# Kernel tuning notes

Hardware: AMD Instinct MI355X
Metric: run time of the kernel (lower is better)

Reference implementation:

```python
import jax, jax.numpy as jnp
import numpy as np

# sigmas (defaults from the module)
VAR_0, VAR_A, VAR_B = 1.0, 1.0, 0.0

def V_phi(a, b, c):
    # default id_phi: (a, b, c) -> b, where Sigma = [[a, b], [b, c]]
    return b


def setup_inputs() -> dict:
    key = jax.random.key(0)
    kx, ky = jax.random.split(key)
    B, T, D = 128, 1024, 64
    dt = 1.0 / (T - 1)
    scale = np.sqrt(dt / D).astype(np.float32)
    # Brownian-like paths: increments ~ N(0, dt/D) so quadratic variation is O(1)
    # and the multiplicative kernel recurrence stays numerically bounded.
    X = jnp.cumsum(jax.random.normal(kx, (B, T, D), jnp.float32) * scale, axis=1)
    Y = jnp.cumsum(jax.random.normal(ky, (B, T, D), jnp.float32) * scale, axis=1)
    return {"X": X, "Y": Y}


def _kernel_same(dd):
    # dd: (b, T-1) = <dX_t, dX_t> / dt ; returns Kxx: (b, T)
    def step(k, d_t):
        k_new = k + (VAR_A * V_phi(k, k, k) + VAR_B) * d_t
        return k_new, k_new
    k0 = jnp.full((dd.shape[0],), VAR_0, dd.dtype)
    _, ks = jax.lax.scan(step, k0, dd.T)           # ks: (T-1, b)
    return jnp.concatenate([k0[None, :], ks], axis=0).T  # (b, T)


def reference(X, Y):
    bx, T, d = X.shape
    by = Y.shape[0]
    interval = jnp.linspace(0.0, 1.0, T).astype(X.dtype)
    dt = jnp.diff(interval)                         # (T-1,)
    dX = jnp.diff(X, axis=1)                        # (bx, T-1, d)
    dY = jnp.diff(Y, axis=1)                        # (by, T-1, d)

    dXdX = (dX * dX).sum(-1) / dt                   # (bx, T-1)
    dYdY = (dY * dY).sum(-1) / dt                   # (by, T-1)
    dXdY = jnp.einsum('itd,jtd->ijt', dX, dY) / dt  # (bx, by, T-1)

    Kxx = _kernel_same(dXdX)                        # (bx, T)
    Kyy = _kernel_same(dYdY)                        # (by, T)

    def step(k, inp):
        kxx_t, kyy_t, dxy_t = inp                   # (bx,), (by,), (bx, by)
        k_new = k + (VAR_A * V_phi(kxx_t[:, None], k, kyy_t[None, :]) + VAR_B) * dxy_t
        return k_new, k_new

    k0 = jnp.full((bx, by), VAR_0, X.dtype)
    xs = (Kxx[:, :-1].T, Kyy[:, :-1].T, jnp.moveaxis(dXdY, 2, 0))
    _, ks = jax.lax.scan(step, k0, xs)              # (T-1, bx, by)
    K = jnp.concatenate([k0[None], ks], axis=0)     # (T, bx, by)
    return jnp.moveaxis(K, 0, 2)                    # (bx, by, T)
```

## Files before the change

### kernel.cpp

```cpp
#include <hip/hip_runtime.h>
#include <hip/hip_bf16.h>

typedef __attribute__((ext_vector_type(8))) short short8;
typedef __attribute__((ext_vector_type(4))) float floatx4;

constexpr int BX    = 128;
constexpr int TT    = 1024;
constexpr int DDIM  = 64;
constexpr int NPAIR = BX * BX;
constexpr int LCH   = 16;
constexpr int NCH   = TT / LCH;
constexpr float DT_INV = 1023.0f;

__device__ __forceinline__ int sidxE(int row, int k) {
    return row * 64 + ((((k >> 3) ^ (row & 7)) << 3) | (k & 7));
}

__device__ __forceinline__ ushort f2bf(float f) {
    uint u = __builtin_bit_cast(uint, f);
    u += 0x7fffu + ((u >> 16) & 1u);
    return (ushort)(u >> 16);
}

__device__ __forceinline__ void cvt_store(ushort* hiP, ushort* loP, const float* v) {
    uint hw[4], lw[4];
#pragma unroll
    for (int p = 0; p < 4; ++p) {
        const __hip_bfloat162 h = __float22bfloat162_rn(make_float2(v[2 * p], v[2 * p + 1]));
        const float r0 = v[2 * p]     - __bfloat162float(h.x);
        const float r1 = v[2 * p + 1] - __bfloat162float(h.y);
        const __hip_bfloat162 l = __float22bfloat162_rn(make_float2(r0, r1));
        hw[p] = (uint)__bfloat16_as_ushort(h.x) | ((uint)__bfloat16_as_ushort(h.y) << 16);
        lw[p] = (uint)__bfloat16_as_ushort(l.x) | ((uint)__bfloat16_as_ushort(l.y) << 16);
    }
    *(uint4*)hiP = make_uint4(hw[0], hw[1], hw[2], hw[3]);
    *(uint4*)loP = make_uint4(lw[0], lw[1], lw[2], lw[3]);
}

__device__ __forceinline__ void ld8(const float* p, float* dst) {
    const float4 a = *(const float4*)p;
    const float4 b = *(const float4*)(p + 4);
    dst[0] = a.x; dst[1] = a.y; dst[2] = a.z; dst[3] = a.w;
    dst[4] = b.x; dst[5] = b.y; dst[6] = b.z; dst[7] = b.w;
}

template<int WP>
__global__ __launch_bounds__(256, 2) void zchunk_kernel(const float* __restrict__ X,
                                                        const float* __restrict__ Y,
                                                        float* __restrict__ dstF,
                                                        uint*  __restrict__ Wp,
                                                        float* __restrict__ P)
{
    __shared__ __align__(16) ushort smXhi[2][64 * 64], smXlo[2][64 * 64];
    __shared__ __align__(16) ushort smYhi[2][32 * 64], smYlo[2][32 * 64];

    const int L    = (int)blockIdx.x;
    const int tile = (L >> 3) & 7;
    const int cz   = ((L >> 6) << 3) | (L & 7);
    const int i0 = (tile & 1) * 64;
    const int j0 = (tile >> 1) * 32;
    const int t0 = cz * LCH;
    const int tid  = (int)threadIdx.x;
    const int lane = tid & 63, w = tid >> 6, quad = lane >> 4, l15 = lane & 15;

    const int srow = tid >> 3;
    const int sseg = tid & 7;
    const float* xp0 = X + (size_t)(i0 + srow)      * TT * DDIM + sseg * 8;
    const float* xp1 = X + (size_t)(i0 + srow + 32) * TT * DDIM + sseg * 8;
    const float* yp  = Y + (size_t)(j0 + srow)      * TT * DDIM + sseg * 8;

    float cx0[8], cx1[8], cy[8];
    float rx0[4][8], rx1[4][8], ry[4][8];
    {
        const int sa = (t0 == 0) ? 0 : (t0 - 1);
        float pv0[8], pv1[8], pv2[8], d[8];
        ld8(xp0 + (size_t)t0 * DDIM, cx0);
        ld8(xp1 + (size_t)t0 * DDIM, cx1);
        ld8(yp  + (size_t)t0 * DDIM, cy);
        ld8(xp0 + (size_t)sa * DDIM, pv0);
        ld8(xp1 + (size_t)sa * DDIM, pv1);
        ld8(yp  + (size_t)sa * DDIM, pv2);
#pragma unroll
        for (int s = 1; s <= 3; ++s) {
            ld8(xp0 + (size_t)(t0 + s) * DDIM, rx0[s]);
            ld8(xp1 + (size_t)(t0 + s) * DDIM, rx1[s]);
            ld8(yp  + (size_t)(t0 + s) * DDIM, ry[s]);
        }

#pragma unroll
        for (int k = 0; k < 8; ++k) d[k] = cx0[k] - pv0[k];
        cvt_store(&smXhi[0][sidxE(srow, sseg * 8)], &smXlo[0][sidxE(srow, sseg * 8)], d);
#pragma unroll
        for (int k = 0; k < 8; ++k) d[k] = cx1[k] - pv1[k];
        cvt_store(&smXhi[0][sidxE(srow + 32, sseg * 8)], &smXlo[0][sidxE(srow + 32, sseg * 8)], d);
#pragma unroll
        for (int k = 0; k < 8; ++k) d[k] = cy[k] - pv2[k];
        cvt_store(&smYhi[0][sidxE(srow, sseg * 8)], &smYlo[0][sidxE(srow, sseg * 8)], d);
    }

    float cum[2][4];
    uint  histP[2][4][8];
#pragma unroll
    for (int s = 0; s < 2; ++s)
#pragma unroll
        for (int r = 0; r < 4; ++r) cum[s][r] = 1.f;

    __syncthreads();

#pragma unroll
    for (int h = 0; h < LCH; ++h) {
        const int cur = h & 1;

        if (h + 4 < LCH) {
            const size_t u = (size_t)(t0 + h + 4) * DDIM;
            ld8(xp0 + u, rx0[h & 3]); ld8(xp1 + u, rx1[h & 3]); ld8(yp + u, ry[h & 3]);
        }

        short8 aHi[2], aLo[2];
#pragma unroll
        for (int kk = 0; kk < 2; ++kk) {
            const int e = sidxE(w * 16 + l15, kk * 32 + quad * 8);
            aHi[kk] = *(const short8*)&smXhi[cur][e];
            aLo[kk] = *(const short8*)&smXlo[cur][e];
        }

#pragma unroll
        for (int sub = 0; sub < 2; ++sub) {
            floatx4 acc = {0.f, 0.f, 0.f, 0.f};
#pragma unroll
            for (int kk = 0; kk < 2; ++kk) {
                const int e = sidxE(sub * 16 + l15, kk * 32 + quad * 8);
                const short8 bHi = *(const short8*)&smYhi[cur][e];
                const short8 bLo = *(const short8*)&smYlo[cur][e];
                acc = __builtin_amdgcn_mfma_f32_16x16x32_bf16(aLo[kk], bHi, acc, 0, 0, 0);
                acc = __builtin_amdgcn_mfma_f32_16x16x32_bf16(aHi[kk], bLo, acc, 0, 0, 0);
                acc = __builtin_amdgcn_mfma_f32_16x16x32_bf16(aHi[kk], bHi, acc, 0, 0, 0);
            }
#pragma unroll
            for (int r = 0; r < 4; ++r) {
                cum[sub][r] *= fmaf(acc[r], DT_INV, 1.f);
                const uint hb = (uint)f2bf(cum[sub][r]);
                if ((h & 1) == 0) histP[sub][r][h >> 1] = hb;
                else              histP[sub][r][h >> 1] |= (hb << 16);
            }
        }

        if (h + 1 < LCH) {
            const int nsel = (h + 1) & 3;
            float d[8];
#pragma unroll
            for (int k = 0; k < 8; ++k) d[k] = rx0[nsel][k] - cx0[k];
            cvt_store(&smXhi[cur ^ 1][sidxE(srow, sseg * 8)], &smXlo[cur ^ 1][sidxE(srow, sseg * 8)], d);
#pragma unroll
            for (int k = 0; k < 8; ++k) d[k] = rx1[nsel][k] - cx1[k];
            cvt_store(&smXhi[cur ^ 1][sidxE(srow + 32, sseg * 8)], &smXlo[cur ^ 1][sidxE(srow + 32, sseg * 8)], d);
#pragma unroll
            for (int k = 0; k < 8; ++k) d[k] = ry[nsel][k] - cy[k];
            cvt_store(&smYhi[cur ^ 1][sidxE(srow, sseg * 8)], &smYlo[cur ^ 1][sidxE(srow, sseg * 8)], d);
#pragma unroll
            for (int k = 0; k < 8; ++k) { cx0[k] = rx0[nsel][k]; cx1[k] = rx1[nsel][k]; cy[k] = ry[nsel][k]; }
            __syncthreads();
        }
    }

#pragma unroll
    for (int sub = 0; sub < 2; ++sub)
#pragma unroll
        for (int r = 0; r < 4; ++r) {
            const int pair = (i0 + w * 16 + quad * 4 + r) * BX + (j0 + sub * 16 + l15);
            P[(size_t)cz * NPAIR + pair] = cum[sub][r];
            if (WP) {
                uint* o = Wp + ((size_t)cz * NPAIR + pair) * 8;
                *(uint4*)o       = make_uint4(histP[sub][r][0], histP[sub][r][1],
                                              histP[sub][r][2], histP[sub][r][3]);
                *(uint4*)(o + 4) = make_uint4(histP[sub][r][4], histP[sub][r][5],
                                              histP[sub][r][6], histP[sub][r][7]);
            } else {
                float* o = dstF + (size_t)pair * TT + t0;
#pragma unroll
                for (int q = 0; q < 4; ++q) {
                    const uint u0 = histP[sub][r][2 * q];
                    const uint u1 = histP[sub][r][2 * q + 1];
                    *(float4*)(o + q * 4) = make_float4(
                        __builtin_bit_cast(float, u0 << 16),
                        __builtin_bit_cast(float, u0 & 0xffff0000u),
                        __builtin_bit_cast(float, u1 << 16),
                        __builtin_bit_cast(float, u1 & 0xffff0000u));
                }
            }
        }
}

__global__ __launch_bounds__(256) void scanscale_w(float* __restrict__ out,
                                                   const uint* __restrict__ W,
                                                   const float* __restrict__ P)
{
    __shared__ uint2 tileW[NCH * 65];
    __shared__ float pf[NCH][17];
    __shared__ float tot[16][17];

    const int p0  = (int)blockIdx.x * 16;
    const int tid = (int)threadIdx.x;
    const int p   = tid & 15;
    const int seg = tid >> 4;

    float v[4], e[4];
#pragma unroll
    for (int k = 0; k < 4; ++k)
        v[k] = P[(size_t)(seg * 4 + k) * NPAIR + p0 + p];
    e[0] = 1.f;
#pragma unroll
    for (int k = 1; k < 4; ++k) e[k] = e[k - 1] * v[k - 1];
    tot[seg][p] = e[3] * v[3];
    __syncthreads();

    float base = 1.f;
#pragma unroll
    for (int q = 0; q < 15; ++q)
        if (q < seg) base *= tot[q][p];
#pragma unroll
    for (int k = 0; k < 4; ++k)
        pf[seg * 4 + k][p] = base * e[k];

    const int wv = tid >> 6, l = tid & 63;
    const int pr = l >> 2, tb = l & 3;
#pragma unroll
    for (int k = 0; k < 16; ++k) {
        const int c = wv * 16 + k;
        tileW[c * 65 + pr * 4 + tb] =
            *(const uint2*)(W + ((size_t)c * NPAIR + p0 + pr) * 8 + tb * 2);
    }
    __syncthreads();

    const int c2 = tid >> 2, q2 = tid & 3;
#pragma unroll 2
    for (int r = 0; r < 16; ++r) {
        const uint2 u = tileW[c2 * 65 + r * 4 + q2];
        const float f = pf[c2][r];
        *(float4*)(out + (size_t)(p0 + r) * TT + tid * 4) = make_float4(
            __builtin_bit_cast(float, u.x << 16) * f,
            __builtin_bit_cast(float, u.x & 0xffff0000u) * f,
            __builtin_bit_cast(float, u.y << 16) * f,
            __builtin_bit_cast(float, u.y & 0xffff0000u) * f);
    }
}

__global__ __launch_bounds__(256) void scanscale_kernel(float* __restrict__ out,
                                                        const float* __restrict__ P)
{
    __shared__ float pf[16][NCH];
    const int p0  = (int)blockIdx.x * 16;
    const int tid = (int)threadIdx.x;

    if (tid < 16) {
        const int p = p0 + tid;
        float run = 1.f;
#pragma unroll 4
        for (int c = 0; c < NCH; ++c) {
            pf[tid][c] = run;
            run *= P[(size_t)c * NPAIR + p];
        }
    }
    __syncthreads();

    const int pp  = tid >> 4;
    const int col = tid & 15;
    float* row = out + (size_t)(p0 + pp) * TT;
#pragma unroll
    for (int seg = 0; seg < 16; ++seg) {
        const int t = seg * 64 + col * 4;
        const float f = pf[pp][t >> 4];
        float4 v = *(float4*)(row + t);
        v.x *= f; v.y *= f; v.z *= f; v.w *= f;
        *(float4*)(row + t) = v;
    }
}

extern "C" void kernel_launch(void* const* d_in, const int* in_sizes, int n_in,
                              void* d_out, int out_size, void* d_ws, size_t ws_size,
                              hipStream_t stream)
{
    const float* X = (const float*)d_in[0];
    const float* Y = (const float*)d_in[1];
    float* out = (float*)d_out;
    float* P   = (float*)d_ws;
    uint*  W   = (uint*)((float*)d_ws + (size_t)NCH * NPAIR);

    const size_t need = (size_t)NCH * NPAIR * (4 + 32);
    if (ws_size >= need) {
        zchunk_kernel<1><<<dim3(512), 256, 0, stream>>>(X, Y, out, W, P);
        scanscale_w<<<dim3(NPAIR / 16), 256, 0, stream>>>(out, W, P);
    } else {
        zchunk_kernel<0><<<dim3(512), 256, 0, stream>>>(X, Y, out, W, P);
        scanscale_kernel<<<dim3(NPAIR / 16), 256, 0, stream>>>(out, P);
    }
}
```

Baseline: 149.0 us.

## Split chunk kernel into single-wave 16x16 tiles without block barriers

Replaces the 256-thread chunk kernel computing 64x32 pair tiles with a one-wavefront kernel computing 16x16 tiles, launched as 4096 blocks. With one wave per block the LDS double buffer no longer needs __syncthreads, and the prefetch depth drops from 4 to 2 steps to save registers. The aim is more parallel blocks and no barrier stalls, at the cost of less reuse of the X/Y increments per tile and so more global/L2 traffic.

```diff
diff --git a/kernel.cpp b/kernel.cpp
--- a/kernel.cpp
+++ b/kernel.cpp
@@ -45,150 +45,152 @@
 }
 
 template<int WP>
-__global__ __launch_bounds__(256, 2) void zchunk_kernel(const float* __restrict__ X,
-                                                        const float* __restrict__ Y,
-                                                        float* __restrict__ dstF,
-                                                        uint*  __restrict__ Wp,
-                                                        float* __restrict__ P)
-{
-    __shared__ __align__(16) ushort smXhi[2][64 * 64], smXlo[2][64 * 64];
-    __shared__ __align__(16) ushort smYhi[2][32 * 64], smYlo[2][32 * 64];
+__global__ __launch_bounds__(64, 2) void zchunk1w(const float* __restrict__ X,
+                                                  const float* __restrict__ Y,
+                                                  float* __restrict__ dstF,
+                                                  uint*  __restrict__ Wp,
+                                                  float* __restrict__ P)
+{
+    __shared__ __align__(16) ushort smXhi[2][16 * 64], smXlo[2][16 * 64];
+    __shared__ __align__(16) ushort smYhi[2][16 * 64], smYlo[2][16 * 64];
 
     const int L    = (int)blockIdx.x;
-    const int tile = (L >> 3) & 7;
-    const int cz   = ((L >> 6) << 3) | (L & 7);
-    const int i0 = (tile & 1) * 64;
-    const int j0 = (tile >> 1) * 32;
+    const int tile = (L >> 3) & 63;
+    const int cz   = ((L >> 9) << 3) | (L & 7);
+    const int i0 = (tile & 7) * 16;
+    const int j0 = (tile >> 3) * 16;
     const int t0 = cz * LCH;
-    const int tid  = (int)threadIdx.x;
-    const int lane = tid & 63, w = tid >> 6, quad = lane >> 4, l15 = lane & 15;
-
-    const int srow = tid >> 3;
-    const int sseg = tid & 7;
-    const float* xp0 = X + (size_t)(i0 + srow)      * TT * DDIM + sseg * 8;
-    const float* xp1 = X + (size_t)(i0 + srow + 32) * TT * DDIM + sseg * 8;
-    const float* yp  = Y + (size_t)(j0 + srow)      * TT * DDIM + sseg * 8;
-
-    float cx0[8], cx1[8], cy[8];
-    float rx0[4][8], rx1[4][8], ry[4][8];
+    const int lane = (int)threadIdx.x;
+    const int quad = lane >> 4, l15 = lane & 15;
+
+    const int srow = lane >> 3;
+    const int sseg = lane & 7;
+    const float* gx0 = X + (size_t)(i0 + srow)     * TT * DDIM + sseg * 8;
+    const float* gx1 = X + (size_t)(i0 + srow + 8) * TT * DDIM + sseg * 8;
+    const float* gy0 = Y + (size_t)(j0 + srow)     * TT * DDIM + sseg * 8;
+    const float* gy1 = Y + (size_t)(j0 + srow + 8) * TT * DDIM + sseg * 8;
+
+    const int eA = sidxE(srow,     sseg * 8);
+    const int eB = sidxE(srow + 8, sseg * 8);
+
+    float cx0[8], cx1[8], cy0[8], cy1[8];
+    float rx0[2][8], rx1[2][8], ry0[2][8], ry1[2][8];
     {
         const int sa = (t0 == 0) ? 0 : (t0 - 1);
-        float pv0[8], pv1[8], pv2[8], d[8];
-        ld8(xp0 + (size_t)t0 * DDIM, cx0);
-        ld8(xp1 + (size_t)t0 * DDIM, cx1);
-        ld8(yp  + (size_t)t0 * DDIM, cy);
-        ld8(xp0 + (size_t)sa * DDIM, pv0);
-        ld8(xp1 + (size_t)sa * DDIM, pv1);
-        ld8(yp  + (size_t)sa * DDIM, pv2);
-#pragma unroll
-        for (int s = 1; s <= 3; ++s) {
-            ld8(xp0 + (size_t)(t0 + s) * DDIM, rx0[s]);
-            ld8(xp1 + (size_t)(t0 + s) * DDIM, rx1[s]);
-            ld8(yp  + (size_t)(t0 + s) * DDIM, ry[s]);
-        }
-
-#pragma unroll
-        for (int k = 0; k < 8; ++k) d[k] = cx0[k] - pv0[k];
-        cvt_store(&smXhi[0][sidxE(srow, sseg * 8)], &smXlo[0][sidxE(srow, sseg * 8)], d);
-#pragma unroll
-        for (int k = 0; k < 8; ++k) d[k] = cx1[k] - pv1[k];
-        cvt_store(&smXhi[0][sidxE(srow + 32, sseg * 8)], &smXlo[0][sidxE(srow + 32, sseg * 8)], d);
-#pragma unroll
-        for (int k = 0; k < 8; ++k) d[k] = cy[k] - pv2[k];
-        cvt_store(&smYhi[0][sidxE(srow, sseg * 8)], &smYlo[0][sidxE(srow, sseg * 8)], d);
-    }
-
-    float cum[2][4];
-    uint  histP[2][4][8];
-#pragma unroll
-    for (int s = 0; s < 2; ++s)
-#pragma unroll
-        for (int r = 0; r < 4; ++r) cum[s][r] = 1.f;
-
-    __syncthreads();
+        float p0[8], p1[8], p2[8], p3[8], d[8];
+        ld8(gx0 + (size_t)t0 * DDIM, cx0);
+        ld8(gx1 + (size_t)t0 * DDIM, cx1);
+        ld8(gy0 + (size_t)t0 * DDIM, cy0);
+        ld8(gy1 + (size_t)t0 * DDIM, cy1);
+        ld8(gx0 + (size_t)sa * DDIM, p0);
+        ld8(gx1 + (size_t)sa * DDIM, p1);
+        ld8(gy0 + (size_t)sa * DDIM, p2);
+        ld8(gy1 + (size_t)sa * DDIM, p3);
+        ld8(gx0 + (size_t)(t0 + 1) * DDIM, rx0[1]);
+        ld8(gx1 + (size_t)(t0 + 1) * DDIM, rx1[1]);
+        ld8(gy0 + (size_t)(t0 + 1) * DDIM, ry0[1]);
+        ld8(gy1 + (size_t)(t0 + 1) * DDIM, ry1[1]);
+
+#pragma unroll
+        for (int k = 0; k < 8; ++k) d[k] = cx0[k] - p0[k];
+        cvt_store(&smXhi[0][eA], &smXlo[0][eA], d);
+#pragma unroll
+        for (int k = 0; k < 8; ++k) d[k] = cx1[k] - p1[k];
+        cvt_store(&smXhi[0][eB], &smXlo[0][eB], d);
+#pragma unroll
+        for (int k = 0; k < 8; ++k) d[k] = cy0[k] - p2[k];
+        cvt_store(&smYhi[0][eA], &smYlo[0][eA], d);
+#pragma unroll
+        for (int k = 0; k < 8; ++k) d[k] = cy1[k] - p3[k];
+        cvt_store(&smYhi[0][eB], &smYlo[0][eB], d);
+    }
+
+    float cum[4];
+    uint  histP[4][8];
+#pragma unroll
+    for (int r = 0; r < 4; ++r) cum[r] = 1.f;
 
 #pragma unroll
     for (int h = 0; h < LCH; ++h) {
         const int cur = h & 1;
 
-        if (h + 4 < LCH) {
-            const size_t u = (size_t)(t0 + h + 4) * DDIM;
-            ld8(xp0 + u, rx0[h & 3]); ld8(xp1 + u, rx1[h & 3]); ld8(yp + u, ry[h & 3]);
-        }
-
-        short8 aHi[2], aLo[2];
+        if (h + 2 < LCH) {
+            const size_t u = (size_t)(t0 + h + 2) * DDIM;
+            ld8(gx0 + u, rx0[h & 1]); ld8(gx1 + u, rx1[h & 1]);
+            ld8(gy0 + u, ry0[h & 1]); ld8(gy1 + u, ry1[h & 1]);
+        }
+
+        short8 aHi[2], aLo[2], bHi[2], bLo[2];
 #pragma unroll
         for (int kk = 0; kk < 2; ++kk) {
-            const int e = sidxE(w * 16 + l15, kk * 32 + quad * 8);
+            const int e = sidxE(l15, kk * 32 + quad * 8);
             aHi[kk] = *(const short8*)&smXhi[cur][e];
             aLo[kk] = *(const short8*)&smXlo[cur][e];
-        }
-
-#pragma unroll
-        for (int sub = 0; sub < 2; ++sub) {
-            floatx4 acc = {0.f, 0.f, 0.f, 0.f};
-#pragma unroll
-            for (int kk = 0; kk < 2; ++kk) {
-                const int e = sidxE(sub * 16 + l15, kk * 32 + quad * 8);
-                const short8 bHi = *(const short8*)&smYhi[cur][e];
-                const short8 bLo = *(const short8*)&smYlo[cur][e];
-                acc = __builtin_amdgcn_mfma_f32_16x16x32_bf16(aLo[kk], bHi, acc, 0, 0, 0);
-                acc = __builtin_amdgcn_mfma_f32_16x16x32_bf16(aHi[kk], bLo, acc, 0, 0, 0);
-                acc = __builtin_amdgcn_mfma_f32_16x16x32_bf16(aHi[kk], bHi, acc, 0, 0, 0);
+            bHi[kk] = *(const short8*)&smYhi[cur][e];
+            bLo[kk] = *(const short8*)&smYlo[cur][e];
+        }
+
+        floatx4 acc = {0.f, 0.f, 0.f, 0.f};
+#pragma unroll
+        for (int kk = 0; kk < 2; ++kk) {
+            acc = __builtin_amdgcn_mfma_f32_16x16x32_bf16(aLo[kk], bHi[kk], acc, 0, 0, 0);
+            acc = __builtin_amdgcn_mfma_f32_16x16x32_bf16(aHi[kk], bLo[kk], acc, 0, 0, 0);
+            acc = __builtin_amdgcn_mfma_f32_16x16x32_bf16(aHi[kk], bHi[kk], acc, 0, 0, 0);
+        }
+#pragma unroll
+        for (int r = 0; r < 4; ++r) {
+            cum[r] *= fmaf(acc[r], DT_INV, 1.f);
+            const uint hb = (uint)f2bf(cum[r]);
+            if ((h & 1) == 0) histP[r][h >> 1] = hb;
+            else              histP[r][h >> 1] |= (hb << 16);
+        }
+
+        if (h + 1 < LCH) {
+            const int nsel = (h + 1) & 1;
+            const int nb   = cur ^ 1;
+            float d[8];
+#pragma unroll
+            for (int k = 0; k < 8; ++k) d[k] = rx0[nsel][k] - cx0[k];
+            cvt_store(&smXhi[nb][eA], &smXlo[nb][eA], d);
+#pragma unroll
+            for (int k = 0; k < 8; ++k) d[k] = rx1[nsel][k] - cx1[k];
+            cvt_store(&smXhi[nb][eB], &smXlo[nb][eB], d);
+#pragma unroll
+            for (int k = 0; k < 8; ++k) d[k] = ry0[nsel][k] - cy0[k];
+            cvt_store(&smYhi[nb][eA], &smYlo[nb][eA], d);
+#pragma unroll
+            for (int k = 0; k < 8; ++k) d[k] = ry1[nsel][k] - cy1[k];
+            cvt_store(&smYhi[nb][eB], &smYlo[nb][eB], d);
+#pragma unroll
+            for (int k = 0; k < 8; ++k) {
+                cx0[k] = rx0[nsel][k]; cx1[k] = rx1[nsel][k];
+                cy0[k] = ry0[nsel][k]; cy1[k] = ry1[nsel][k];
             }
-#pragma unroll
-            for (int r = 0; r < 4; ++r) {
-                cum[sub][r] *= fmaf(acc[r], DT_INV, 1.f);
-                const uint hb = (uint)f2bf(cum[sub][r]);
-                if ((h & 1) == 0) histP[sub][r][h >> 1] = hb;
-                else              histP[sub][r][h >> 1] |= (hb << 16);
+        }
+    }
+
+#pragma unroll
+    for (int r = 0; r < 4; ++r) {
+        const int pair = (i0 + quad * 4 + r) * BX + (j0 + l15);
+        P[(size_t)cz * NPAIR + pair] = cum[r];
+        if (WP) {
+            uint* o = Wp + ((size_t)cz * NPAIR + pair) * 8;
+            *(uint4*)o       = make_uint4(histP[r][0], histP[r][1], histP[r][2], histP[r][3]);
+            *(uint4*)(o + 4) = make_uint4(histP[r][4], histP[r][5], histP[r][6], histP[r][7]);
+        } else {
+            float* o = dstF + (size_t)pair * TT + t0;
+#pragma unroll
+            for (int q = 0; q < 4; ++q) {
+                const uint u0 = histP[r][2 * q];
+                const uint u1 = histP[r][2 * q + 1];
+                *(float4*)(o + q * 4) = make_float4(
+                    __builtin_bit_cast(float, u0 << 16),
+                    __builtin_bit_cast(float, u0 & 0xffff0000u),
+                    __builtin_bit_cast(float, u1 << 16),
+                    __builtin_bit_cast(float, u1 & 0xffff0000u));
             }
         }
-
-        if (h + 1 < LCH) {
-            const int nsel = (h + 1) & 3;
-            float d[8];
-#pragma unroll
-            for (int k = 0; k < 8; ++k) d[k] = rx0[nsel][k] - cx0[k];
-            cvt_store(&smXhi[cur ^ 1][sidxE(srow, sseg * 8)], &smXlo[cur ^ 1][sidxE(srow, sseg * 8)], d);
-#pragma unroll
-            for (int k = 0; k < 8; ++k) d[k] = rx1[nsel][k] - cx1[k];
-            cvt_store(&smXhi[cur ^ 1][sidxE(srow + 32, sseg * 8)], &smXlo[cur ^ 1][sidxE(srow + 32, sseg * 8)], d);
-#pragma unroll
-            for (int k = 0; k < 8; ++k) d[k] = ry[nsel][k] - cy[k];
-            cvt_store(&smYhi[cur ^ 1][sidxE(srow, sseg * 8)], &smYlo[cur ^ 1][sidxE(srow, sseg * 8)], d);
-#pragma unroll
-            for (int k = 0; k < 8; ++k) { cx0[k] = rx0[nsel][k]; cx1[k] = rx1[nsel][k]; cy[k] = ry[nsel][k]; }
-            __syncthreads();
-        }
-    }
-
-#pragma unroll
-    for (int sub = 0; sub < 2; ++sub)
-#pragma unroll
-        for (int r = 0; r < 4; ++r) {
-            const int pair = (i0 + w * 16 + quad * 4 + r) * BX + (j0 + sub * 16 + l15);
-            P[(size_t)cz * NPAIR + pair] = cum[sub][r];
-            if (WP) {
-                uint* o = Wp + ((size_t)cz * NPAIR + pair) * 8;
-                *(uint4*)o       = make_uint4(histP[sub][r][0], histP[sub][r][1],
-                                              histP[sub][r][2], histP[sub][r][3]);
-                *(uint4*)(o + 4) = make_uint4(histP[sub][r][4], histP[sub][r][5],
-                                              histP[sub][r][6], histP[sub][r][7]);
-            } else {
-                float* o = dstF + (size_t)pair * TT + t0;
-#pragma unroll
-                for (int q = 0; q < 4; ++q) {
-                    const uint u0 = histP[sub][r][2 * q];
-                    const uint u1 = histP[sub][r][2 * q + 1];
-                    *(float4*)(o + q * 4) = make_float4(
-                        __builtin_bit_cast(float, u0 << 16),
-                        __builtin_bit_cast(float, u0 & 0xffff0000u),
-                        __builtin_bit_cast(float, u1 << 16),
-                        __builtin_bit_cast(float, u1 & 0xffff0000u));
-                }
-            }
-        }
+    }
 }
 
 __global__ __launch_bounds__(256) void scanscale_w(float* __restrict__ out,
@@ -288,10 +290,10 @@
 
     const size_t need = (size_t)NCH * NPAIR * (4 + 32);
     if (ws_size >= need) {
-        zchunk_kernel<1><<<dim3(512), 256, 0, stream>>>(X, Y, out, W, P);
+        zchunk1w<1><<<dim3(4096), 64, 0, stream>>>(X, Y, out, W, P);
         scanscale_w<<<dim3(NPAIR / 16), 256, 0, stream>>>(out, W, P);
     } else {
-        zchunk_kernel<0><<<dim3(512), 256, 0, stream>>>(X, Y, out, W, P);
+        zchunk1w<0><<<dim3(4096), 64, 0, stream>>>(X, Y, out, W, P);
         scanscale_kernel<<<dim3(NPAIR / 16), 256, 0, stream>>>(out, P);
     }
 }
```

Result: slower. 170.8 us (+14.6%).
